# Kernel tuning notes

Measured on AMD Instinct MI355X. Metric: run time of the kernel, lower is better.

The kernel has to match this reference:

```python
import jax, jax.numpy as jnp
import numpy as np
import math

B, S_IN, S_OUT, D_IN, D_OUT, G = 8, 1024, 1024, 96, 96, 8
LN_EPS = 1e-5


def setup_inputs() -> dict:
    key = jax.random.key(0)
    k_x, k_m, k_p, k_l = jax.random.split(key, 4)
    x = jax.random.normal(k_x, (B, S_IN, D_IN), dtype=jnp.float32)
    M = jax.random.uniform(k_m, (D_OUT, D_IN), minval=-0.5, maxval=0.5, dtype=jnp.float32)
    P = jax.random.uniform(k_p, (D_OUT, D_OUT, G), minval=-0.1, maxval=0.1, dtype=jnp.float32)
    Linker = jax.random.uniform(k_l, (S_IN, S_OUT), minval=-0.1, maxval=0.1, dtype=jnp.float32)
    gamma = jnp.ones((D_OUT,), dtype=jnp.float32)
    beta = jnp.zeros((D_OUT,), dtype=jnp.float32)
    return {"x": x, "M": M, "P": P, "Linker": Linker, "gamma": gamma, "beta": beta}


def _layer_norm(z, gamma, beta):
    mu = jnp.mean(z, axis=-1, keepdims=True)
    var = jnp.mean(jnp.square(z - mu), axis=-1, keepdims=True)
    return (z - mu) * jax.lax.rsqrt(var + LN_EPS) * gamma + beta


def reference(x, M, P, Linker, gamma, beta):
    # Z = x @ M^T, then LayerNorm over feature dim
    Z0 = jnp.einsum('bsj,ij->bsi', x, M)           # (B, S_in, D_out)
    Z = _layer_norm(Z0, gamma, beta)
    # periods[i,j,g] = i*(D_out*G) + j*G + g + 2
    periods = (jnp.arange(D_OUT * D_OUT * G, dtype=jnp.float32)
               .reshape(D_OUT, D_OUT, G) + 2.0)
    k = jnp.arange(S_IN, dtype=jnp.float32)
    # phi[s,i,j,g] = cos(2*pi*s / periods[i,j,g])
    phi = jnp.cos((2.0 * math.pi) * k[:, None, None, None] / periods[None])
    # fuse basis reduction: W[s,i,j] = sum_g P[i,j,g] * phi[s,i,j,g]
    W = jnp.einsum('sijg,ijg->sij', phi, P)        # (S_in, D_out, D_out)
    # T[b,s,i] = sum_j Z[b,s,j] * W[s,i,j]
    T = jnp.einsum('bsj,sij->bsi', Z, W)           # (B, S_in, D_out)
    # sequence transform via Linker
    U = jnp.einsum('bsi,st->bti', T, Linker)       # (B, S_out, D_out)
    # shared residual: x @ M^T (pre-LN) through the same Linker
    residual = jnp.einsum('bsi,st->bti', Z0, Linker)
    return U + residual
```

## Files before the change

### kernel.cpp

```cpp
#include <hip/hip_runtime.h>
#include <hip/hip_bf16.h>
#include <cstdint>
#include <cstddef>

#define NB 8
#define NS 1024
#define ND 96
#define NPAIR (ND*ND)
#define BSTRIDE (NS*ND)

typedef __attribute__((ext_vector_type(8))) short short8;
typedef __attribute__((ext_vector_type(4))) float f32x4;

__device__ __forceinline__ uint16_t f2bf(float x) {
    uint32_t u = __float_as_uint(x);
    uint32_t r = (u + 0x7FFF + ((u >> 16) & 1)) >> 16;
    return (uint16_t)r;
}
__device__ __forceinline__ float bf2f(uint16_t b) {
    uint32_t u = ((uint32_t)b) << 16;
    return __uint_as_float(u);
}

union SmemK1 {
    float M[96][97];
    struct { float zb[16][100]; float ps[16][6][2]; float stats[16][2]; } ln;
    struct { float T[64][65]; } kl;
};

__global__ __launch_bounds__(96) void k1_mega(
    const float* __restrict__ x, const float* __restrict__ M,
    const float* __restrict__ P, const float* __restrict__ L,
    const float* __restrict__ gamma, const float* __restrict__ beta,
    float* __restrict__ Z0, float* __restrict__ Z,
    uint16_t* __restrict__ Lt, uint16_t* __restrict__ Wt)
{
    __shared__ SmemK1 sm;
    const int t  = threadIdx.x;
    const int bx = blockIdx.x;

    if (bx < 512) {
        const int R0 = bx * 16;
        for (int k = 0; k < 24; ++k) {
            int mm = t + 96 * k;
            int i = mm / 24, j0 = (mm % 24) * 4;
            float4 v = *(const float4*)(M + i * 96 + j0);
            sm.M[i][j0]   = v.x; sm.M[i][j0+1] = v.y;
            sm.M[i][j0+2] = v.z; sm.M[i][j0+3] = v.w;
        }
        __syncthreads();
        float mreg[96];
        #pragma unroll
        for (int j = 0; j < 96; ++j) mreg[j] = sm.M[t][j];
        __syncthreads();

        for (int r = 0; r < 16; ++r) {
            const float* xr = x + (size_t)(R0 + r) * 96;
            float a0 = 0.f, a1 = 0.f, a2 = 0.f, a3 = 0.f;
            #pragma unroll
            for (int j = 0; j < 96; j += 4) {
                a0 = fmaf(xr[j+0], mreg[j+0], a0);
                a1 = fmaf(xr[j+1], mreg[j+1], a1);
                a2 = fmaf(xr[j+2], mreg[j+2], a2);
                a3 = fmaf(xr[j+3], mreg[j+3], a3);
            }
            float z = (a0 + a1) + (a2 + a3);
            sm.ln.zb[r][t] = z;
            Z0[(size_t)(R0 + r) * 96 + t] = z;
        }
        __syncthreads();
        {
            const int row = t / 6, seg = t % 6;
            const float4* zp = (const float4*)&sm.ln.zb[row][seg * 16];
            float s1 = 0.f, s2 = 0.f;
            #pragma unroll
            for (int k = 0; k < 4; ++k) {
                float4 v = zp[k];
                s1 += v.x + v.y + v.z + v.w;
                s2 += v.x*v.x + v.y*v.y + v.z*v.z + v.w*v.w;
            }
            sm.ln.ps[row][seg][0] = s1;
            sm.ln.ps[row][seg][1] = s2;
        }
        __syncthreads();
        if (t < 16) {
            float s1 = 0.f, s2 = 0.f;
            #pragma unroll
            for (int k = 0; k < 6; ++k) {
                s1 += sm.ln.ps[t][k][0];
                s2 += sm.ln.ps[t][k][1];
            }
            float mu  = s1 * (1.f / 96.f);
            float var = s2 * (1.f / 96.f) - mu * mu;
            sm.ln.stats[t][0] = mu;
            sm.ln.stats[t][1] = rsqrtf(var + 1e-5f);
        }
        __syncthreads();
        {
            float gm = gamma[t], bt = beta[t];
            for (int r = 0; r < 16; ++r) {
                float mu = sm.ln.stats[r][0], rs = sm.ln.stats[r][1];
                Z[(size_t)(R0 + r) * 96 + t] =
                    (sm.ln.zb[r][t] - mu) * rs * gm + bt;
            }
        }
        return;
    }

    if (bx < 768) {
        const int bx2 = bx - 512;
        const int s0 = (bx2 & 15) * 64, t0 = (bx2 >> 4) * 64;
        if (t < 64) {
            for (int r = 0; r < 64; ++r)
                sm.kl.T[r][t] = L[(size_t)(s0 + r) * 1024 + t0 + t];
        }
        __syncthreads();
        if (t < 64) {
            uint16_t* orow = Lt + (size_t)(t0 + t) * 1024 + s0;
            #pragma unroll
            for (int c4 = 0; c4 < 16; ++c4) {
                uint32_t u01 = (uint32_t)f2bf(sm.kl.T[c4*4+0][t]) |
                               ((uint32_t)f2bf(sm.kl.T[c4*4+1][t]) << 16);
                uint32_t u23 = (uint32_t)f2bf(sm.kl.T[c4*4+2][t]) |
                               ((uint32_t)f2bf(sm.kl.T[c4*4+3][t]) << 16);
                uint2 o; o.x = u01; o.y = u23;
                *(uint2*)(orow + c4 * 4) = o;
            }
        }
        return;
    }

    {
        const int idx = bx - 768;
        const int pb  = idx % 96;
        const int sc  = idx / 96;
        const int p   = pb * 96 + t;
        const int s0  = sc * 64;
        const int base = p * 8;

        float Pv[8], c[8], cp[8], tc1[8];
        {
            float4 a = *(const float4*)(P + base);
            float4 b = *(const float4*)(P + base + 4);
            Pv[0]=a.x; Pv[1]=a.y; Pv[2]=a.z; Pv[3]=a.w;
            Pv[4]=b.x; Pv[5]=b.y; Pv[6]=b.z; Pv[7]=b.w;
        }
        #pragma unroll
        for (int g = 0; g < 8; ++g) {
            float pf  = (float)(base + g + 2);
            float inv = 1.0f / pf;
            float c1  = cospif(2.0f * inv);
            tc1[g] = c1 + c1;
            c[g]  = cospif(2.0f * (float)s0 * inv);
            cp[g] = cospif(2.0f * (float)(s0 - 1) * inv);
        }
        uint16_t* op = Wt + (size_t)s0 * NPAIR + p;
        for (int ss = 0; ss < 64; ++ss) {
            float w = 0.f;
            #pragma unroll
            for (int g = 0; g < 8; ++g) w = fmaf(Pv[g], c[g], w);
            *op = f2bf(w);
            op += NPAIR;
            #pragma unroll
            for (int g = 0; g < 8; ++g) {
                float cn = fmaf(tc1[g], c[g], -cp[g]);
                cp[g] = c[g]; c[g] = cn;
            }
        }
    }
}

__global__ __launch_bounds__(96) void kt_apply(
    const float* __restrict__ Z, const float* __restrict__ Z0,
    const uint16_t* __restrict__ Wt, uint16_t* __restrict__ Vt)
{
    const int i = threadIdx.x;
    const int s = blockIdx.x;
    float acc[8] = {0.f,0.f,0.f,0.f,0.f,0.f,0.f,0.f};
    const uint16_t* wrow = Wt + (size_t)s * NPAIR + i * 96;
    const float* zs = Z + (size_t)s * 96;
    for (int j0 = 0; j0 < 96; j0 += 8) {
        short8 w8 = *(const short8*)(wrow + j0);
        float w[8];
        #pragma unroll
        for (int jj = 0; jj < 8; ++jj) w[jj] = bf2f((uint16_t)w8[jj]);
        #pragma unroll
        for (int bb = 0; bb < 8; ++bb) {
            const float* zb = zs + (size_t)bb * BSTRIDE + j0;
            #pragma unroll
            for (int jj = 0; jj < 8; ++jj)
                acc[bb] = fmaf(zb[jj], w[jj], acc[bb]);
        }
    }
    #pragma unroll
    for (int bb = 0; bb < 8; ++bb) {
        size_t o = (size_t)bb * BSTRIDE + (size_t)s * 96 + i;
        Vt[((size_t)bb * 96 + i) * 1024 + s] = f2bf(acc[bb] + Z0[o]);
    }
}

__global__ __launch_bounds__(128) void k3_mfma(
    const uint16_t* __restrict__ Lt, const uint16_t* __restrict__ Vt,
    float* __restrict__ out)
{
    const int lane = threadIdx.x & 63;
    const int wv   = threadIdx.x >> 6;
    const int m    = lane & 15;
    const int quad = lane >> 4;
    const int t0   = blockIdx.x * 32 + wv * 16;
    const int b    = blockIdx.y;

    const uint16_t* Lp = Lt + (size_t)(t0 + m) * 1024 + quad * 8;
    const uint16_t* Vp = Vt + ((size_t)b * 96 + m) * 1024 + quad * 8;

    f32x4 acc[6];
    #pragma unroll
    for (int ii = 0; ii < 6; ++ii) acc[ii] = (f32x4){0.f, 0.f, 0.f, 0.f};

    short8 a = *(const short8*)Lp;
    short8 bv[6];
    #pragma unroll
    for (int ii = 0; ii < 6; ++ii)
        bv[ii] = *(const short8*)(Vp + (size_t)ii * 16 * 1024);

    for (int kc = 0; kc < 31; ++kc) {
        short8 an = *(const short8*)(Lp + (kc + 1) * 32);
        short8 bn[6];
        #pragma unroll
        for (int ii = 0; ii < 6; ++ii)
            bn[ii] = *(const short8*)(Vp + (size_t)ii * 16 * 1024 + (kc + 1) * 32);
        #pragma unroll
        for (int ii = 0; ii < 6; ++ii)
            acc[ii] = __builtin_amdgcn_mfma_f32_16x16x32_bf16(a, bv[ii], acc[ii], 0, 0, 0);
        a = an;
        #pragma unroll
        for (int ii = 0; ii < 6; ++ii) bv[ii] = bn[ii];
    }
    #pragma unroll
    for (int ii = 0; ii < 6; ++ii)
        acc[ii] = __builtin_amdgcn_mfma_f32_16x16x32_bf16(a, bv[ii], acc[ii], 0, 0, 0);

    float* po = out + (size_t)b * BSTRIDE;
    #pragma unroll
    for (int ii = 0; ii < 6; ++ii)
        #pragma unroll
        for (int r = 0; r < 4; ++r)
            po[(size_t)(t0 + quad * 4 + r) * 96 + ii * 16 + m] = acc[ii][r];
}

extern "C" void kernel_launch(void* const* d_in, const int* in_sizes, int n_in,
                              void* d_out, int out_size, void* d_ws, size_t ws_size,
                              hipStream_t stream)
{
    const float* x     = (const float*)d_in[0];
    const float* M     = (const float*)d_in[1];
    const float* P     = (const float*)d_in[2];
    const float* Lnk   = (const float*)d_in[3];
    const float* gamma = (const float*)d_in[4];
    const float* beta  = (const float*)d_in[5];
    float* out = (float*)d_out;

    uint8_t* ws = (uint8_t*)d_ws;
    uint16_t* Wt  = (uint16_t*)ws;
    float*    Z0  = (float*)(ws + 18874368);
    float*    Z   = (float*)(ws + 22020096);
    uint16_t* Lt  = (uint16_t*)(ws + 25165824);
    uint16_t* Vt  = (uint16_t*)(ws + 27262976);

    k1_mega <<<2304, 96, 0, stream>>>(x, M, P, Lnk, gamma, beta, Z0, Z, Lt, Wt);
    kt_apply<<<1024, 96, 0, stream>>>(Z, Z0, Wt, Vt);
    k3_mfma <<<dim3(32, 8), 128, 0, stream>>>(Lt, Vt, out);
}
```

Before: 125.8 us.

## Fuse three kernels into one cooperative persistent kernel with grid syncs

Replaces the three-kernel pipeline with a single cooperative kernel of 256 blocks of 256 threads that runs the precompute, apply and Linker-GEMM phases separated by grid.sync, and falls back to three launches if the cooperative launch fails. Each phase's work distribution is remapped to the fixed grid: 128 blocks do projection+LayerNorm, 16 blocks transpose Linker, 112 blocks generate W with grid-stride loops. The MFMA GEMM now splits K across two waves and reduces the halves through shared memory. The aim is to remove launch overhead and gaps between kernels, at the cost of much lower parallelism in phase 1 and the cost of the grid-wide barriers.

```diff
diff --git a/kernel.cpp b/kernel.cpp
--- a/kernel.cpp
+++ b/kernel.cpp
@@ -1,217 +1,209 @@
 #include <hip/hip_runtime.h>
-#include <hip/hip_bf16.h>
+#include <hip/hip_cooperative_groups.h>
 #include <cstdint>
 #include <cstddef>
 
-#define NB 8
-#define NS 1024
-#define ND 96
-#define NPAIR (ND*ND)
-#define BSTRIDE (NS*ND)
+namespace cg = cooperative_groups;
+
+#define NPAIR 9216
+#define BSTRIDE 98304
 
 typedef __attribute__((ext_vector_type(8))) short short8;
 typedef __attribute__((ext_vector_type(4))) float f32x4;
 
 __device__ __forceinline__ uint16_t f2bf(float x) {
     uint32_t u = __float_as_uint(x);
-    uint32_t r = (u + 0x7FFF + ((u >> 16) & 1)) >> 16;
-    return (uint16_t)r;
+    return (uint16_t)((u + 0x7FFF + ((u >> 16) & 1)) >> 16);
 }
 __device__ __forceinline__ float bf2f(uint16_t b) {
-    uint32_t u = ((uint32_t)b) << 16;
-    return __uint_as_float(u);
-}
-
-union SmemK1 {
-    float M[96][97];
-    struct { float zb[16][100]; float ps[16][6][2]; float stats[16][2]; } ln;
-    struct { float T[64][65]; } kl;
+    return __uint_as_float(((uint32_t)b) << 16);
+}
+
+union Smem {
+    struct { float zb[2][32][100]; float ps[2][32][3][2]; float stats[2][32][2]; } ln;
+    struct { float T[64][17]; } kl;
+    struct { float red[2][2][64][25]; } r3;
 };
 
-__global__ __launch_bounds__(96) void k1_mega(
+__device__ void phase1(Smem& sm, int bx, int t,
     const float* __restrict__ x, const float* __restrict__ M,
     const float* __restrict__ P, const float* __restrict__ L,
     const float* __restrict__ gamma, const float* __restrict__ beta,
     float* __restrict__ Z0, float* __restrict__ Z,
     uint16_t* __restrict__ Lt, uint16_t* __restrict__ Wt)
 {
-    __shared__ SmemK1 sm;
-    const int t  = threadIdx.x;
-    const int bx = blockIdx.x;
-
-    if (bx < 512) {
-        const int R0 = bx * 16;
-        for (int k = 0; k < 24; ++k) {
-            int mm = t + 96 * k;
-            int i = mm / 24, j0 = (mm % 24) * 4;
-            float4 v = *(const float4*)(M + i * 96 + j0);
-            sm.M[i][j0]   = v.x; sm.M[i][j0+1] = v.y;
-            sm.M[i][j0+2] = v.z; sm.M[i][j0+3] = v.w;
+    if (bx < 128) {
+        const int g = t >> 7, lt = t & 127;
+        const int R0 = bx * 64 + g * 32;
+        if (lt < 96) {
+            float mreg[96];
+            #pragma unroll
+            for (int k4 = 0; k4 < 24; ++k4) {
+                float4 v = *(const float4*)(M + lt * 96 + k4 * 4);
+                mreg[k4*4+0]=v.x; mreg[k4*4+1]=v.y;
+                mreg[k4*4+2]=v.z; mreg[k4*4+3]=v.w;
+            }
+            for (int r = 0; r < 32; ++r) {
+                const float* xr = x + (size_t)(R0 + r) * 96;
+                float a0 = 0.f, a1 = 0.f, a2 = 0.f, a3 = 0.f;
+                #pragma unroll
+                for (int j = 0; j < 96; j += 4) {
+                    a0 = fmaf(xr[j+0], mreg[j+0], a0);
+                    a1 = fmaf(xr[j+1], mreg[j+1], a1);
+                    a2 = fmaf(xr[j+2], mreg[j+2], a2);
+                    a3 = fmaf(xr[j+3], mreg[j+3], a3);
+                }
+                float z = (a0 + a1) + (a2 + a3);
+                sm.ln.zb[g][r][lt] = z;
+                Z0[(size_t)(R0 + r) * 96 + lt] = z;
+            }
         }
         __syncthreads();
-        float mreg[96];
-        #pragma unroll
-        for (int j = 0; j < 96; ++j) mreg[j] = sm.M[t][j];
+        if (lt < 96) {
+            int row = lt / 3, seg = lt % 3;
+            const float4* zp = (const float4*)&sm.ln.zb[g][row][seg * 32];
+            float s1 = 0.f, s2 = 0.f;
+            #pragma unroll
+            for (int k = 0; k < 8; ++k) {
+                float4 v = zp[k];
+                s1 += (v.x + v.y) + (v.z + v.w);
+                s2 += (v.x*v.x + v.y*v.y) + (v.z*v.z + v.w*v.w);
+            }
+            sm.ln.ps[g][row][seg][0] = s1;
+            sm.ln.ps[g][row][seg][1] = s2;
+        }
         __syncthreads();
-
-        for (int r = 0; r < 16; ++r) {
-            const float* xr = x + (size_t)(R0 + r) * 96;
-            float a0 = 0.f, a1 = 0.f, a2 = 0.f, a3 = 0.f;
-            #pragma unroll
-            for (int j = 0; j < 96; j += 4) {
-                a0 = fmaf(xr[j+0], mreg[j+0], a0);
-                a1 = fmaf(xr[j+1], mreg[j+1], a1);
-                a2 = fmaf(xr[j+2], mreg[j+2], a2);
-                a3 = fmaf(xr[j+3], mreg[j+3], a3);
-            }
-            float z = (a0 + a1) + (a2 + a3);
-            sm.ln.zb[r][t] = z;
-            Z0[(size_t)(R0 + r) * 96 + t] = z;
-        }
-        __syncthreads();
-        {
-            const int row = t / 6, seg = t % 6;
-            const float4* zp = (const float4*)&sm.ln.zb[row][seg * 16];
-            float s1 = 0.f, s2 = 0.f;
-            #pragma unroll
-            for (int k = 0; k < 4; ++k) {
-                float4 v = zp[k];
-                s1 += v.x + v.y + v.z + v.w;
-                s2 += v.x*v.x + v.y*v.y + v.z*v.z + v.w*v.w;
-            }
-            sm.ln.ps[row][seg][0] = s1;
-            sm.ln.ps[row][seg][1] = s2;
-        }
-        __syncthreads();
-        if (t < 16) {
-            float s1 = 0.f, s2 = 0.f;
-            #pragma unroll
-            for (int k = 0; k < 6; ++k) {
-                s1 += sm.ln.ps[t][k][0];
-                s2 += sm.ln.ps[t][k][1];
-            }
+        if (lt < 32) {
+            float s1 = sm.ln.ps[g][lt][0][0] + sm.ln.ps[g][lt][1][0] + sm.ln.ps[g][lt][2][0];
+            float s2 = sm.ln.ps[g][lt][0][1] + sm.ln.ps[g][lt][1][1] + sm.ln.ps[g][lt][2][1];
             float mu  = s1 * (1.f / 96.f);
             float var = s2 * (1.f / 96.f) - mu * mu;
-            sm.ln.stats[t][0] = mu;
-            sm.ln.stats[t][1] = rsqrtf(var + 1e-5f);
+            sm.ln.stats[g][lt][0] = mu;
+            sm.ln.stats[g][lt][1] = rsqrtf(var + 1e-5f);
         }
         __syncthreads();
-        {
-            float gm = gamma[t], bt = beta[t];
-            for (int r = 0; r < 16; ++r) {
-                float mu = sm.ln.stats[r][0], rs = sm.ln.stats[r][1];
-                Z[(size_t)(R0 + r) * 96 + t] =
-                    (sm.ln.zb[r][t] - mu) * rs * gm + bt;
-            }
-        }
-        return;
-    }
-
-    if (bx < 768) {
-        const int bx2 = bx - 512;
-        const int s0 = (bx2 & 15) * 64, t0 = (bx2 >> 4) * 64;
-        if (t < 64) {
-            for (int r = 0; r < 64; ++r)
-                sm.kl.T[r][t] = L[(size_t)(s0 + r) * 1024 + t0 + t];
-        }
-        __syncthreads();
-        if (t < 64) {
-            uint16_t* orow = Lt + (size_t)(t0 + t) * 1024 + s0;
-            #pragma unroll
-            for (int c4 = 0; c4 < 16; ++c4) {
-                uint32_t u01 = (uint32_t)f2bf(sm.kl.T[c4*4+0][t]) |
-                               ((uint32_t)f2bf(sm.kl.T[c4*4+1][t]) << 16);
-                uint32_t u23 = (uint32_t)f2bf(sm.kl.T[c4*4+2][t]) |
-                               ((uint32_t)f2bf(sm.kl.T[c4*4+3][t]) << 16);
-                uint2 o; o.x = u01; o.y = u23;
-                *(uint2*)(orow + c4 * 4) = o;
-            }
-        }
-        return;
-    }
-
-    {
-        const int idx = bx - 768;
-        const int pb  = idx % 96;
-        const int sc  = idx / 96;
-        const int p   = pb * 96 + t;
-        const int s0  = sc * 64;
-        const int base = p * 8;
-
-        float Pv[8], c[8], cp[8], tc1[8];
-        {
-            float4 a = *(const float4*)(P + base);
-            float4 b = *(const float4*)(P + base + 4);
-            Pv[0]=a.x; Pv[1]=a.y; Pv[2]=a.z; Pv[3]=a.w;
-            Pv[4]=b.x; Pv[5]=b.y; Pv[6]=b.z; Pv[7]=b.w;
-        }
-        #pragma unroll
-        for (int g = 0; g < 8; ++g) {
-            float pf  = (float)(base + g + 2);
-            float inv = 1.0f / pf;
-            float c1  = cospif(2.0f * inv);
-            tc1[g] = c1 + c1;
-            c[g]  = cospif(2.0f * (float)s0 * inv);
-            cp[g] = cospif(2.0f * (float)(s0 - 1) * inv);
-        }
-        uint16_t* op = Wt + (size_t)s0 * NPAIR + p;
-        for (int ss = 0; ss < 64; ++ss) {
-            float w = 0.f;
-            #pragma unroll
-            for (int g = 0; g < 8; ++g) w = fmaf(Pv[g], c[g], w);
-            *op = f2bf(w);
-            op += NPAIR;
+        if (lt < 96) {
+            float gm = gamma[lt], bt = beta[lt];
+            for (int r = 0; r < 32; ++r) {
+                float mu = sm.ln.stats[g][r][0], rs = sm.ln.stats[g][r][1];
+                Z[(size_t)(R0 + r) * 96 + lt] = (sm.ln.zb[g][r][lt] - mu) * rs * gm + bt;
+            }
+        }
+    } else if (bx < 144) {
+        for (int cgi = 0; cgi < 4; ++cgi) {
+            const int t0 = (bx - 128) * 64 + cgi * 16;
+            const int tx = t & 15, ty = t >> 4;
+            for (int s0 = 0; s0 < 1024; s0 += 64) {
+                #pragma unroll
+                for (int k = 0; k < 4; ++k) {
+                    int sr = ty + k * 16;
+                    sm.kl.T[sr][tx] = L[(size_t)(s0 + sr) * 1024 + t0 + tx];
+                }
+                __syncthreads();
+                {
+                    int trow = t >> 4, sc = (t & 15) * 4;
+                    uint32_t u01 = (uint32_t)f2bf(sm.kl.T[sc+0][trow]) |
+                                   ((uint32_t)f2bf(sm.kl.T[sc+1][trow]) << 16);
+                    uint32_t u23 = (uint32_t)f2bf(sm.kl.T[sc+2][trow]) |
+                                   ((uint32_t)f2bf(sm.kl.T[sc+3][trow]) << 16);
+                    uint2 o; o.x = u01; o.y = u23;
+                    *(uint2*)(Lt + (size_t)(t0 + trow) * 1024 + s0 + sc) = o;
+                }
+                __syncthreads();
+            }
+        }
+    } else {
+        for (int u = (bx - 144) * 256 + t; u < 36864; u += 112 * 256) {
+            const int p  = u % 9216;
+            const int s0 = (u / 9216) * 256;
+            const int base = p * 8;
+            float Pv[8], inv[8], tc1[8], c[8], cp[8];
+            {
+                float4 a = *(const float4*)(P + base);
+                float4 b = *(const float4*)(P + base + 4);
+                Pv[0]=a.x; Pv[1]=a.y; Pv[2]=a.z; Pv[3]=a.w;
+                Pv[4]=b.x; Pv[5]=b.y; Pv[6]=b.z; Pv[7]=b.w;
+            }
             #pragma unroll
             for (int g = 0; g < 8; ++g) {
-                float cn = fmaf(tc1[g], c[g], -cp[g]);
-                cp[g] = c[g]; c[g] = cn;
-            }
-        }
-    }
-}
-
-__global__ __launch_bounds__(96) void kt_apply(
+                inv[g] = 1.0f / (float)(base + g + 2);
+                float c1 = cospif(2.0f * inv[g]);
+                tc1[g] = c1 + c1;
+            }
+            for (int half = 0; half < 2; ++half) {
+                const int sh = s0 + half * 128;
+                #pragma unroll
+                for (int g = 0; g < 8; ++g) {
+                    c[g]  = cospif(2.0f * (float)sh * inv[g]);
+                    cp[g] = cospif(2.0f * (float)(sh - 1) * inv[g]);
+                }
+                uint16_t* op = Wt + (size_t)sh * NPAIR + p;
+                for (int ss = 0; ss < 128; ++ss) {
+                    float w = 0.f;
+                    #pragma unroll
+                    for (int g = 0; g < 8; ++g) w = fmaf(Pv[g], c[g], w);
+                    *op = f2bf(w);
+                    op += NPAIR;
+                    #pragma unroll
+                    for (int g = 0; g < 8; ++g) {
+                        float cn = fmaf(tc1[g], c[g], -cp[g]);
+                        cp[g] = c[g]; c[g] = cn;
+                    }
+                }
+            }
+        }
+    }
+}
+
+__device__ void phase2(int bx, int t,
     const float* __restrict__ Z, const float* __restrict__ Z0,
     const uint16_t* __restrict__ Wt, uint16_t* __restrict__ Vt)
 {
-    const int i = threadIdx.x;
-    const int s = blockIdx.x;
-    float acc[8] = {0.f,0.f,0.f,0.f,0.f,0.f,0.f,0.f};
-    const uint16_t* wrow = Wt + (size_t)s * NPAIR + i * 96;
-    const float* zs = Z + (size_t)s * 96;
-    for (int j0 = 0; j0 < 96; j0 += 8) {
-        short8 w8 = *(const short8*)(wrow + j0);
-        float w[8];
-        #pragma unroll
-        for (int jj = 0; jj < 8; ++jj) w[jj] = bf2f((uint16_t)w8[jj]);
+    const int g = t >> 7, lt = t & 127;
+    if (lt >= 96) return;
+    const int i = lt;
+    for (int it = 0; it < 2; ++it) {
+        const int s = bx * 4 + g * 2 + it;
+        float acc[8] = {0.f,0.f,0.f,0.f,0.f,0.f,0.f,0.f};
+        const uint16_t* wrow = Wt + (size_t)s * NPAIR + i * 96;
+        const float* zs = Z + (size_t)s * 96;
+        for (int j0 = 0; j0 < 96; j0 += 8) {
+            short8 w8 = *(const short8*)(wrow + j0);
+            float w[8];
+            #pragma unroll
+            for (int jj = 0; jj < 8; ++jj) w[jj] = bf2f((uint16_t)w8[jj]);
+            #pragma unroll
+            for (int bb = 0; bb < 8; ++bb) {
+                const float* zbp = zs + (size_t)bb * BSTRIDE + j0;
+                #pragma unroll
+                for (int jj = 0; jj < 8; ++jj)
+                    acc[bb] = fmaf(zbp[jj], w[jj], acc[bb]);
+            }
+        }
         #pragma unroll
         for (int bb = 0; bb < 8; ++bb) {
-            const float* zb = zs + (size_t)bb * BSTRIDE + j0;
-            #pragma unroll
-            for (int jj = 0; jj < 8; ++jj)
-                acc[bb] = fmaf(zb[jj], w[jj], acc[bb]);
-        }
-    }
-    #pragma unroll
-    for (int bb = 0; bb < 8; ++bb) {
-        size_t o = (size_t)bb * BSTRIDE + (size_t)s * 96 + i;
-        Vt[((size_t)bb * 96 + i) * 1024 + s] = f2bf(acc[bb] + Z0[o]);
-    }
-}
-
-__global__ __launch_bounds__(128) void k3_mfma(
+            size_t o = (size_t)bb * BSTRIDE + (size_t)s * 96 + i;
+            Vt[((size_t)bb * 96 + i) * 1024 + s] = f2bf(acc[bb] + Z0[o]);
+        }
+    }
+}
+
+__device__ void phase3(Smem& sm, int bx, int t,
     const uint16_t* __restrict__ Lt, const uint16_t* __restrict__ Vt,
     float* __restrict__ out)
 {
-    const int lane = threadIdx.x & 63;
-    const int wv   = threadIdx.x >> 6;
+    const int lane = t & 63;
+    const int wv   = t >> 6;
+    const int p    = wv >> 1;
+    const int h    = wv & 1;
     const int m    = lane & 15;
     const int quad = lane >> 4;
-    const int t0   = blockIdx.x * 32 + wv * 16;
-    const int b    = blockIdx.y;
-
-    const uint16_t* Lp = Lt + (size_t)(t0 + m) * 1024 + quad * 8;
-    const uint16_t* Vp = Vt + ((size_t)b * 96 + m) * 1024 + quad * 8;
+    const int tid  = bx * 2 + p;
+    const int t0   = (tid >> 3) * 16;
+    const int b    = tid & 7;
+
+    const uint16_t* Lp = Lt + (size_t)(t0 + m) * 1024 + h * 512 + quad * 8;
+    const uint16_t* Vp = Vt + ((size_t)b * 96 + m) * 1024 + h * 512 + quad * 8;
 
     f32x4 acc[6];
     #pragma unroll
@@ -223,7 +215,7 @@
     for (int ii = 0; ii < 6; ++ii)
         bv[ii] = *(const short8*)(Vp + (size_t)ii * 16 * 1024);
 
-    for (int kc = 0; kc < 31; ++kc) {
+    for (int kc = 0; kc < 15; ++kc) {
         short8 an = *(const short8*)(Lp + (kc + 1) * 32);
         short8 bn[6];
         #pragma unroll
@@ -240,12 +232,65 @@
     for (int ii = 0; ii < 6; ++ii)
         acc[ii] = __builtin_amdgcn_mfma_f32_16x16x32_bf16(a, bv[ii], acc[ii], 0, 0, 0);
 
-    float* po = out + (size_t)b * BSTRIDE;
     #pragma unroll
     for (int ii = 0; ii < 6; ++ii)
         #pragma unroll
         for (int r = 0; r < 4; ++r)
-            po[(size_t)(t0 + quad * 4 + r) * 96 + ii * 16 + m] = acc[ii][r];
+            sm.r3.red[p][h][lane][ii * 4 + r] = acc[ii][r];
+    __syncthreads();
+    {
+        const int p2 = t >> 7, sub = (t >> 6) & 1, l2 = t & 63;
+        const int m2 = l2 & 15, q2 = l2 >> 4;
+        const int tid2 = bx * 2 + p2;
+        const int t02 = (tid2 >> 3) * 16, b2 = tid2 & 7;
+        #pragma unroll
+        for (int k = sub * 12; k < sub * 12 + 12; ++k) {
+            float sv = sm.r3.red[p2][0][l2][k] + sm.r3.red[p2][1][l2][k];
+            int ii = k >> 2, r = k & 3;
+            out[(size_t)b2 * BSTRIDE + (size_t)(t02 + q2 * 4 + r) * 96 + ii * 16 + m2] = sv;
+        }
+    }
+}
+
+__global__ __launch_bounds__(256, 2) void mega(
+    const float* __restrict__ x, const float* __restrict__ M,
+    const float* __restrict__ P, const float* __restrict__ L,
+    const float* __restrict__ gamma, const float* __restrict__ beta,
+    float* __restrict__ Z0, float* __restrict__ Z,
+    uint16_t* __restrict__ Lt, uint16_t* __restrict__ Wt,
+    uint16_t* __restrict__ Vt, float* __restrict__ out)
+{
+    cg::grid_group grid = cg::this_grid();
+    __shared__ Smem sm;
+    phase1(sm, blockIdx.x, threadIdx.x, x, M, P, L, gamma, beta, Z0, Z, Lt, Wt);
+    grid.sync();
+    phase2(blockIdx.x, threadIdx.x, Z, Z0, Wt, Vt);
+    grid.sync();
+    phase3(sm, blockIdx.x, threadIdx.x, Lt, Vt, out);
+}
+
+__global__ __launch_bounds__(256, 2) void kp1(
+    const float* __restrict__ x, const float* __restrict__ M,
+    const float* __restrict__ P, const float* __restrict__ L,
+    const float* __restrict__ gamma, const float* __restrict__ beta,
+    float* __restrict__ Z0, float* __restrict__ Z,
+    uint16_t* __restrict__ Lt, uint16_t* __restrict__ Wt)
+{
+    __shared__ Smem sm;
+    phase1(sm, blockIdx.x, threadIdx.x, x, M, P, L, gamma, beta, Z0, Z, Lt, Wt);
+}
+__global__ __launch_bounds__(256, 2) void kp2(
+    const float* __restrict__ Z, const float* __restrict__ Z0,
+    const uint16_t* __restrict__ Wt, uint16_t* __restrict__ Vt)
+{
+    phase2(blockIdx.x, threadIdx.x, Z, Z0, Wt, Vt);
+}
+__global__ __launch_bounds__(256, 2) void kp3(
+    const uint16_t* __restrict__ Lt, const uint16_t* __restrict__ Vt,
+    float* __restrict__ out)
+{
+    __shared__ Smem sm;
+    phase3(sm, blockIdx.x, threadIdx.x, Lt, Vt, out);
 }
 
 extern "C" void kernel_launch(void* const* d_in, const int* in_sizes, int n_in,
@@ -261,13 +306,27 @@
     float* out = (float*)d_out;
 
     uint8_t* ws = (uint8_t*)d_ws;
-    uint16_t* Wt  = (uint16_t*)ws;
-    float*    Z0  = (float*)(ws + 18874368);
-    float*    Z   = (float*)(ws + 22020096);
-    uint16_t* Lt  = (uint16_t*)(ws + 25165824);
-    uint16_t* Vt  = (uint16_t*)(ws + 27262976);
-
-    k1_mega <<<2304, 96, 0, stream>>>(x, M, P, Lnk, gamma, beta, Z0, Z, Lt, Wt);
-    kt_apply<<<1024, 96, 0, stream>>>(Z, Z0, Wt, Vt);
-    k3_mfma <<<dim3(32, 8), 128, 0, stream>>>(Lt, Vt, out);
-}
+    uint16_t* Wt = (uint16_t*)ws;
+    float*    Z0 = (float*)(ws + 18874368);
+    float*    Z  = (float*)(ws + 22020096);
+    uint16_t* Lt = (uint16_t*)(ws + 25165824);
+    uint16_t* Vt = (uint16_t*)(ws + 27262976);
+
+    int maxblk = 0;
+    hipError_t qerr = hipOccupancyMaxActiveBlocksPerMultiprocessor(
+        &maxblk, reinterpret_cast<const void*>(&mega), 256, 0);
+    bool coop_done = false;
+    if (qerr == hipSuccess && maxblk >= 1) {
+        void* args[12] = { (void*)&x, (void*)&M, (void*)&P, (void*)&Lnk,
+                           (void*)&gamma, (void*)&beta, (void*)&Z0, (void*)&Z,
+                           (void*)&Lt, (void*)&Wt, (void*)&Vt, (void*)&out };
+        hipError_t lerr = hipLaunchCooperativeKernel(
+            reinterpret_cast<void*>(&mega), dim3(256), dim3(256), args, 0, stream);
+        coop_done = (lerr == hipSuccess);
+    }
+    if (!coop_done) {
+        kp1<<<256, 256, 0, stream>>>(x, M, P, Lnk, gamma, beta, Z0, Z, Lt, Wt);
+        kp2<<<256, 256, 0, stream>>>(Z, Z0, Wt, Vt);
+        kp3<<<256, 256, 0, stream>>>(Lt, Vt, out);
+    }
+}
```

After: 240.8 us. 1.91x slower.
